# Kernel tuning notes

Hardware: AMD Instinct MI355X
Metric: run time of the kernel (lower is better)

The kernel has to match this reference:

```python
import jax, jax.numpy as jnp
import numpy as np

EMBED_DIM = 1024
NUM_HEADS = 16
HEAD_DIM = EMBED_DIM // NUM_HEADS
SCALE = HEAD_DIM ** -0.5


def setup_inputs() -> dict:
    key = jax.random.key(0)
    ks = jax.random.split(key, 9)
    B, N = 2, 2048
    s = EMBED_DIM ** -0.5  # ~ torch Linear init scale
    x = jax.random.normal(ks[0], (B, N, EMBED_DIM), dtype=jnp.float32)
    Wq = jax.random.uniform(ks[1], (EMBED_DIM, EMBED_DIM), jnp.float32, -s, s)
    bq = jax.random.uniform(ks[2], (EMBED_DIM,), jnp.float32, -s, s)
    Wk = jax.random.uniform(ks[3], (EMBED_DIM, EMBED_DIM), jnp.float32, -s, s)
    bk = jax.random.uniform(ks[4], (EMBED_DIM,), jnp.float32, -s, s)
    Wv = jax.random.uniform(ks[5], (EMBED_DIM, EMBED_DIM), jnp.float32, -s, s)
    bv = jax.random.uniform(ks[6], (EMBED_DIM,), jnp.float32, -s, s)
    Wo = jax.random.uniform(ks[7], (EMBED_DIM, EMBED_DIM), jnp.float32, -s, s)
    bo = jax.random.uniform(ks[8], (EMBED_DIM,), jnp.float32, -s, s)
    return {"x": x, "Wq": Wq, "bq": bq, "Wk": Wk, "bk": bk,
            "Wv": Wv, "bv": bv, "Wo": Wo, "bo": bo}


def reference(x, Wq, bq, Wk, bk, Wv, bv, Wo, bo):
    B, N, R = x.shape
    H, D = NUM_HEADS, HEAD_DIM
    # projections: Linear(x) = x @ W^T + b; reshape to (B, H, N, D)
    def proj(W, b):
        return (x @ W.T + b).reshape(B, N, H, D).transpose(0, 2, 1, 3)
    q = proj(Wq, bq)
    k = proj(Wk, bk)
    v = proj(Wv, bv)
    attn = jnp.einsum('bhnd,bhmd->bhnm', q, k) * SCALE  # (B,H,N,N)
    attn = jax.nn.softmax(attn, axis=-1)
    out = jnp.einsum('bhnm,bhmd->bhnd', attn, v)        # (B,H,N,D)
    out = out.transpose(0, 2, 1, 3).reshape(B, N, R)
    return out @ Wo.T + bo
```

## Files before the change

### kernel.cpp

```cpp
#include <hip/hip_runtime.h>
#include <stdint.h>

typedef __bf16 bf16;
typedef __bf16 bf16x4 __attribute__((ext_vector_type(4)));
typedef __bf16 bf16x8 __attribute__((ext_vector_type(8)));
typedef float f32x4 __attribute__((ext_vector_type(4)));

#define MFMA16(a, b, c) __builtin_amdgcn_mfma_f32_16x16x32_bf16((a), (b), (c), 0, 0, 0)

#define EMBED 1024
#define SEQ   2048
#define MROWS 4096
#define ATTN_QSCALE 0.1803368801111f

__device__ __forceinline__ void gl2lds16(const bf16* g, bf16* l) {
    __builtin_amdgcn_global_load_lds(
        (const __attribute__((address_space(1))) void*)g,
        (__attribute__((address_space(3))) void*)l,
        16, 0, 0);
}

__global__ __launch_bounds__(256) void cast_all_kernel(
    const float* __restrict__ x,  const float* __restrict__ Wq,
    const float* __restrict__ Wk, const float* __restrict__ Wv,
    const float* __restrict__ Wo, bf16* __restrict__ dst) {
    const int blk = blockIdx.x;
    const float* src;
    size_t so, dofs;
    if (blk < 2048) {
        src = x; so = (size_t)blk * 2048; dofs = so;
    } else {
        const int w = (blk - 2048) >> 9;
        so  = (size_t)((blk - 2048) & 511) * 2048;
        src = (w == 0) ? Wq : (w == 1) ? Wk : (w == 2) ? Wv : Wo;
        dofs = (size_t)(4 + w) * 1024 * 1024 + so;
    }
    const size_t i = (size_t)threadIdx.x * 8;
    float4 a = *(const float4*)(src + so + i);
    float4 b = *(const float4*)(src + so + i + 4);
    bf16x8 o;
    o[0] = (bf16)a.x; o[1] = (bf16)a.y; o[2] = (bf16)a.z; o[3] = (bf16)a.w;
    o[4] = (bf16)b.x; o[5] = (bf16)b.y; o[6] = (bf16)b.z; o[7] = (bf16)b.w;
    *(bf16x8*)(dst + dofs + i) = o;
}

template <bool SCALE>
__device__ __forceinline__ void gemm_tile(const bf16* __restrict__ A,
                                          const bf16* __restrict__ W,
                                          const float* __restrict__ bias,
                                          bf16* __restrict__ C,
                                          int m0, int n0, bf16* smem) {
    const int lane = threadIdx.x & 63;
    const int wv   = threadIdx.x >> 6;
    const int wm   = (wv >> 1) * 64;
    const int wn   = (wv & 1) * 64;
    const int fr   = lane & 15;
    const int quad = lane >> 4;
    const int srow = wv * 8 + (lane >> 3);
    const int swz  = (((lane & 7) ^ ((lane >> 3) & 7))) * 8;

    f32x4 acc[4][4];
#pragma unroll
    for (int mt = 0; mt < 4; ++mt)
#pragma unroll
        for (int nt = 0; nt < 4; ++nt)
            acc[mt][nt] = (f32x4){0.f, 0.f, 0.f, 0.f};

    auto stage = [&](int kt, int bb) {
        bf16* As = smem + bb * 16384;
        bf16* Bs = As + 8192;
        const int k0 = kt * 64;
#pragma unroll
        for (int i = 0; i < 4; ++i) {
            gl2lds16(A + (size_t)(m0 + i * 32 + srow) * 1024 + k0 + swz,
                     &As[(i * 32 + wv * 8) * 64]);
            gl2lds16(W + (size_t)(n0 + i * 32 + srow) * 1024 + k0 + swz,
                     &Bs[(i * 32 + wv * 8) * 64]);
        }
    };

    stage(0, 0);
#pragma unroll
    for (int kt = 0; kt < 16; ++kt) {
        const int bb = kt & 1;
        asm volatile("s_waitcnt vmcnt(0)" ::: "memory");
        __builtin_amdgcn_s_barrier();
        if (kt < 15) stage(kt + 1, bb ^ 1);
        const bf16* As = smem + bb * 16384;
        const bf16* Bs = As + 8192;
#pragma unroll
        for (int ks = 0; ks < 2; ++ks) {
            const int fcol = ((ks * 4 + quad) ^ (fr & 7)) * 8;
            bf16x8 af[4], bfr[4];
#pragma unroll
            for (int t = 0; t < 4; ++t) {
                af[t]  = *(const bf16x8*)&As[(wm + t * 16 + fr) * 64 + fcol];
                bfr[t] = *(const bf16x8*)&Bs[(wn + t * 16 + fr) * 64 + fcol];
            }
            __builtin_amdgcn_s_setprio(1);
#pragma unroll
            for (int mt = 0; mt < 4; ++mt)
#pragma unroll
                for (int nt = 0; nt < 4; ++nt)
                    acc[mt][nt] = MFMA16(af[mt], bfr[nt], acc[mt][nt]);
            __builtin_amdgcn_s_setprio(0);
        }
    }

    float bv[4];
#pragma unroll
    for (int nt = 0; nt < 4; ++nt)
        bv[nt] = bias[n0 + wn + nt * 16 + fr];
    const int row4 = quad * 4;
#pragma unroll
    for (int mt = 0; mt < 4; ++mt)
#pragma unroll
        for (int nt = 0; nt < 4; ++nt)
#pragma unroll
            for (int r = 0; r < 4; ++r) {
                int m = m0 + wm + mt * 16 + row4 + r;
                int n = n0 + wn + nt * 16 + fr;
                float v = acc[mt][nt][r] + bv[nt];
                if (SCALE) v *= ATTN_QSCALE;
                C[(size_t)m * 1024 + n] = (bf16)v;
            }
}

__device__ __forceinline__ void v_tile(const bf16* __restrict__ x,
                                       const bf16* __restrict__ Wv,
                                       const float* __restrict__ bias,
                                       bf16* __restrict__ VT,
                                       int m0, int n0, bf16* smem) {
    const int lane = threadIdx.x & 63;
    const int wv   = threadIdx.x >> 6;
    const int wmW  = (wv >> 1) * 64;
    const int wnT  = (wv & 1) * 64;
    const int f    = lane & 15;
    const int quad = lane >> 4;
    const int srow = wv * 8 + (lane >> 3);
    const int swz  = (((lane & 7) ^ ((lane >> 3) & 7))) * 8;

    f32x4 acc[4][4];
#pragma unroll
    for (int mt = 0; mt < 4; ++mt)
#pragma unroll
        for (int nt = 0; nt < 4; ++nt)
            acc[mt][nt] = (f32x4){0.f, 0.f, 0.f, 0.f};

    auto stage = [&](int kt, int bb) {
        bf16* As = smem + bb * 16384;
        bf16* Bs = As + 8192;
        const int k0 = kt * 64;
#pragma unroll
        for (int i = 0; i < 4; ++i) {
            gl2lds16(x  + (size_t)(m0 + i * 32 + srow) * 1024 + k0 + swz,
                     &As[(i * 32 + wv * 8) * 64]);
            gl2lds16(Wv + (size_t)(n0 + i * 32 + srow) * 1024 + k0 + swz,
                     &Bs[(i * 32 + wv * 8) * 64]);
        }
    };

    stage(0, 0);
#pragma unroll
    for (int kt = 0; kt < 16; ++kt) {
        const int bb = kt & 1;
        asm volatile("s_waitcnt vmcnt(0)" ::: "memory");
        __builtin_amdgcn_s_barrier();
        if (kt < 15) stage(kt + 1, bb ^ 1);
        const bf16* As = smem + bb * 16384;
        const bf16* Bs = As + 8192;
#pragma unroll
        for (int ks = 0; ks < 2; ++ks) {
            const int fcol = ((ks * 4 + quad) ^ (f & 7)) * 8;
            bf16x8 wf[4], xf[4];
#pragma unroll
            for (int t = 0; t < 4; ++t) {
                wf[t] = *(const bf16x8*)&Bs[(wmW + t * 16 + f) * 64 + fcol];
                xf[t] = *(const bf16x8*)&As[(wnT + t * 16 + f) * 64 + fcol];
            }
            __builtin_amdgcn_s_setprio(1);
#pragma unroll
            for (int mt = 0; mt < 4; ++mt)
#pragma unroll
                for (int nt = 0; nt < 4; ++nt)
                    acc[mt][nt] = MFMA16(wf[mt], xf[nt], acc[mt][nt]);
            __builtin_amdgcn_s_setprio(0);
        }
    }

    float4 b4[4];
#pragma unroll
    for (int mt = 0; mt < 4; ++mt)
        b4[mt] = *(const float4*)&bias[n0 + wmW + mt * 16 + quad * 4];

    __syncthreads();

#pragma unroll
    for (int mt = 0; mt < 4; ++mt)
#pragma unroll
        for (int nt = 0; nt < 4; ++nt) {
            const int tok = wnT + nt * 16 + f;
#pragma unroll
            for (int r = 0; r < 4; ++r) {
                const float bvr = (r == 0) ? b4[mt].x : (r == 1) ? b4[mt].y
                                : (r == 2) ? b4[mt].z : b4[mt].w;
                smem[(wmW + mt * 16 + quad * 4 + r) * 136 + tok] =
                    (bf16)(acc[mt][nt][r] + bvr);
            }
        }
    __syncthreads();

    const int n_r  = threadIdx.x >> 4;
    const int t8   = (threadIdx.x & 15) * 8;
    const int base = t8 & ~31;
    const int u4   = ((t8 >> 3) & 3) * 4;
    const int bb   = m0 >> 11;
    const int tokg = (m0 & 2047) + t8;
#pragma unroll
    for (int p = 0; p < 8; ++p) {
        const int n_loc = p * 16 + n_r;
        const bf16* row = &smem[n_loc * 136];
        bf16x4 a = *(const bf16x4*)&row[base + u4];
        bf16x4 b = *(const bf16x4*)&row[base + 16 + u4];
        bf16x8 v = {a[0], a[1], a[2], a[3], b[0], b[1], b[2], b[3]};
        *(bf16x8*)&VT[((size_t)(bb * 1024 + n0 + n_loc)) * 2048 + tokg] = v;
    }
}

__global__ __launch_bounds__(256) void qkv_kernel(
    const bf16* __restrict__ x,
    const bf16* __restrict__ Wq, const float* __restrict__ bq,
    const bf16* __restrict__ Wk, const float* __restrict__ bk,
    const bf16* __restrict__ Wv, const float* __restrict__ bv,
    bf16* __restrict__ Q, bf16* __restrict__ K, bf16* __restrict__ VT) {
    __shared__ __align__(16) bf16 smem[32768];
    const int m0    = blockIdx.x * 128;
    const int which = blockIdx.y >> 3;
    const int n0    = (blockIdx.y & 7) * 128;
    if (which == 0)      gemm_tile<true>(x, Wq, bq, Q, m0, n0, smem);
    else if (which == 1) gemm_tile<false>(x, Wk, bk, K, m0, n0, smem);
    else                 v_tile(x, Wv, bv, VT, m0, n0, smem);
}

__global__ __launch_bounds__(256) void oproj_kernel(
    const bf16* __restrict__ A, const bf16* __restrict__ W,
    const float* __restrict__ bias, float* __restrict__ C) {
    const int m0 = blockIdx.x * 128;
    const int n0 = blockIdx.y * 64;

    __shared__ __align__(16) bf16 smem[24576];

    const int lane = threadIdx.x & 63;
    const int wv   = threadIdx.x >> 6;
    const int wm   = (wv >> 1) * 64;
    const int wn   = (wv & 1) * 32;
    const int fr   = lane & 15;
    const int quad = lane >> 4;
    const int srow = wv * 8 + (lane >> 3);
    const int swz  = (((lane & 7) ^ ((lane >> 3) & 7))) * 8;

    f32x4 acc[4][2];
#pragma unroll
    for (int mt = 0; mt < 4; ++mt)
#pragma unroll
        for (int nt = 0; nt < 2; ++nt)
            acc[mt][nt] = (f32x4){0.f, 0.f, 0.f, 0.f};

    auto stage = [&](int kt, int bb) {
        bf16* As = smem + bb * 12288;
        bf16* Bs = As + 8192;
        const int k0 = kt * 64;
#pragma unroll
        for (int i = 0; i < 4; ++i)
            gl2lds16(A + (size_t)(m0 + i * 32 + srow) * 1024 + k0 + swz,
                     &As[(i * 32 + wv * 8) * 64]);
#pragma unroll
        for (int i = 0; i < 2; ++i)
            gl2lds16(W + (size_t)(n0 + i * 32 + srow) * 1024 + k0 + swz,
                     &Bs[(i * 32 + wv * 8) * 64]);
    };

    stage(0, 0);
#pragma unroll
    for (int kt = 0; kt < 16; ++kt) {
        const int bb = kt & 1;
        asm volatile("s_waitcnt vmcnt(0)" ::: "memory");
        __builtin_amdgcn_s_barrier();
        if (kt < 15) stage(kt + 1, bb ^ 1);
        const bf16* As = smem + bb * 12288;
        const bf16* Bs = As + 8192;
#pragma unroll
        for (int ks = 0; ks < 2; ++ks) {
            const int fcol = ((ks * 4 + quad) ^ (fr & 7)) * 8;
            bf16x8 af[4], bfr[2];
#pragma unroll
            for (int t = 0; t < 4; ++t)
                af[t] = *(const bf16x8*)&As[(wm + t * 16 + fr) * 64 + fcol];
#pragma unroll
            for (int t = 0; t < 2; ++t)
                bfr[t] = *(const bf16x8*)&Bs[(wn + t * 16 + fr) * 64 + fcol];
            __builtin_amdgcn_s_setprio(1);
#pragma unroll
            for (int mt = 0; mt < 4; ++mt)
#pragma unroll
                for (int nt = 0; nt < 2; ++nt)
                    acc[mt][nt] = MFMA16(af[mt], bfr[nt], acc[mt][nt]);
            __builtin_amdgcn_s_setprio(0);
        }
    }

    float bv[2];
#pragma unroll
    for (int nt = 0; nt < 2; ++nt)
        bv[nt] = bias[n0 + wn + nt * 16 + fr];
    const int row4 = quad * 4;
#pragma unroll
    for (int mt = 0; mt < 4; ++mt)
#pragma unroll
        for (int nt = 0; nt < 2; ++nt)
#pragma unroll
            for (int r = 0; r < 4; ++r) {
                int m = m0 + wm + mt * 16 + row4 + r;
                int n = n0 + wn + nt * 16 + fr;
                C[(size_t)m * 1024 + n] = acc[mt][nt][r] + bv[nt];
            }
}

__global__ __launch_bounds__(256, 2) void attn_kernel(
    const bf16* __restrict__ Q, const bf16* __restrict__ K,
    const bf16* __restrict__ VT, bf16* __restrict__ Opart,
    float* __restrict__ lpart) {
    const int tid  = threadIdx.x;
    const int lane = tid & 63;
    const int wv   = tid >> 6;
    const int quad = lane >> 4;
    const int f    = lane & 15;
    const int qt   = blockIdx.x >> 1;
    const int half = blockIdx.x & 1;
    const int q0   = qt * 256;
    const int kvb  = half * 1024;
    const int b    = blockIdx.y >> 4;
    const int h    = blockIdx.y & 15;

    const bf16* Qp = Q + ((size_t)b * SEQ) * 1024 + (size_t)h * 64;
    const bf16* Kp = K + ((size_t)b * SEQ) * 1024 + (size_t)h * 64;
    const bf16* Vp = VT + ((size_t)(b * 1024 + h * 64)) * 2048;
    bf16*  Op = Opart + (size_t)half * MROWS * 1024
                      + ((size_t)b * SEQ) * 1024 + (size_t)h * 64;
    float* lp = lpart + ((size_t)(half * 2 + b) * 16 + h) * SEQ;

    __shared__ bf16 Ks[4][64 * 64];
    __shared__ bf16 VTs[4][64 * 64];

    bf16x8 qf[4][2];
#pragma unroll
    for (int qg = 0; qg < 4; ++qg) {
        const bf16* qrow = Qp + (size_t)(q0 + wv * 64 + qg * 16 + f) * 1024;
        qf[qg][0] = *(const bf16x8*)(qrow + quad * 8);
        qf[qg][1] = *(const bf16x8*)(qrow + 32 + quad * 8);
    }

    const int srow = wv * 8 + (lane >> 3);
    const int swz  = (((lane & 7) ^ ((lane >> 3) & 7))) * 8;
    auto stageK = [&](int t, int bb) {
        const int kv0 = kvb + t * 64;
#pragma unroll
        for (int i = 0; i < 2; ++i)
            gl2lds16(Kp + (size_t)(kv0 + i * 32 + srow) * 1024 + swz,
                     &Ks[bb][(i * 32 + wv * 8) * 64]);
    };
    auto stageVT = [&](int t, int bb) {
        const int kv0 = kvb + t * 64;
#pragma unroll
        for (int i = 0; i < 2; ++i)
            gl2lds16(Vp + (size_t)(i * 32 + srow) * 2048 + kv0 + swz,
                     &VTs[bb][(i * 32 + wv * 8) * 64]);
    };

    stageK(0, 0); stageVT(0, 0);
    stageK(1, 1); stageVT(1, 1);

    f32x4 oacc[4][4];
#pragma unroll
    for (int qg = 0; qg < 4; ++qg)
#pragma unroll
        for (int t = 0; t < 4; ++t)
            oacc[qg][t] = (f32x4){0.f, 0.f, 0.f, 0.f};
    f32x4 lacc[4];
#pragma unroll
    for (int qg = 0; qg < 4; ++qg)
        lacc[qg] = (f32x4){0.f, 0.f, 0.f, 0.f};
    const bf16x8 ones8 = {(bf16)1.f, (bf16)1.f, (bf16)1.f, (bf16)1.f,
                          (bf16)1.f, (bf16)1.f, (bf16)1.f, (bf16)1.f};
    const f32x4  zero4 = (f32x4){0.f, 0.f, 0.f, 0.f};

    const int fcol0 = (quad ^ (f & 7)) * 8;
    const int fcol1 = ((4 + quad) ^ (f & 7)) * 8;

    auto step = [&](int t, int bb, int drain) {
        if (drain == 8) { stageK(t + 2, (t + 2) & 3); stageVT(t + 2, (t + 2) & 3); }
        if (drain == 8)      asm volatile("s_waitcnt vmcnt(8)" ::: "memory");
        else if (drain == 4) asm volatile("s_waitcnt vmcnt(4)" ::: "memory");
        else                 asm volatile("s_waitcnt vmcnt(0)" ::: "memory");
        __builtin_amdgcn_s_barrier();

        bf16x8 kf0[4], kf1[4];
#pragma unroll
        for (int t4 = 0; t4 < 4; ++t4) {
            kf0[t4] = *(const bf16x8*)&Ks[bb][(t4 * 16 + f) * 64 + fcol0];
            kf1[t4] = *(const bf16x8*)&Ks[bb][(t4 * 16 + f) * 64 + fcol1];
        }
        bf16x8 pb8[4][2];
#pragma unroll
        for (int qg = 0; qg < 4; ++qg) {
            f32x4 s[4];
            __builtin_amdgcn_s_setprio(1);
#pragma unroll
            for (int t4 = 0; t4 < 4; ++t4) {
                s[t4] = MFMA16(kf0[t4], qf[qg][0], zero4);
                s[t4] = MFMA16(kf1[t4], qf[qg][1], s[t4]);
            }
            __builtin_amdgcn_s_setprio(0);
#pragma unroll
            for (int kt = 0; kt < 2; ++kt) {
#pragma unroll
                for (int r = 0; r < 4; ++r) {
                    pb8[qg][kt][r]     = (bf16)__builtin_amdgcn_exp2f(s[2 * kt][r]);
                    pb8[qg][kt][4 + r] = (bf16)__builtin_amdgcn_exp2f(s[2 * kt + 1][r]);
                }
                lacc[qg] = MFMA16(ones8, pb8[qg][kt], lacc[qg]);
            }
        }

        __builtin_amdgcn_s_setprio(1);
#pragma unroll
        for (int dt = 0; dt < 4; ++dt) {
#pragma unroll
            for (int kt = 0; kt < 2; ++kt) {
                const int pc = ((kt * 4 + quad) ^ (f & 7)) * 8;
                bf16x8 vf = *(const bf16x8*)&VTs[bb][(dt * 16 + f) * 64 + pc];
#pragma unroll
                for (int qg = 0; qg < 4; ++qg)
                    oacc[qg][dt] = MFMA16(vf, pb8[qg][kt], oacc[qg][dt]);
            }
        }
        __builtin_amdgcn_s_setprio(0);
    };

    for (int tt = 0; tt < 12; tt += 4) {
        step(tt, 0, 8); step(tt + 1, 1, 8); step(tt + 2, 2, 8); step(tt + 3, 3, 8);
    }
    step(12, 0, 8); step(13, 1, 8); step(14, 2, 4); step(15, 3, 0);

#pragma unroll
    for (int qg = 0; qg < 4; ++qg) {
        const int q = q0 + wv * 64 + qg * 16 + f;
        bf16* orow = Op + (size_t)q * 1024;
#pragma unroll
        for (int dt = 0; dt < 4; ++dt) {
            bf16x4 ov;
#pragma unroll
            for (int r = 0; r < 4; ++r)
                ov[r] = (bf16)oacc[qg][dt][r];
            *(bf16x4*)(orow + dt * 16 + quad * 4) = ov;
        }
        if (quad == 0)
            lp[q] = lacc[qg][0];
    }
}

__global__ __launch_bounds__(256) void combine_kernel(
    const bf16* __restrict__ Opart, const float* __restrict__ lpart,
    bf16* __restrict__ O) {
    const int gid = blockIdx.x * 256 + threadIdx.x;
    const int row = gid >> 7;
    const int c8  = (gid & 127) * 8;
    const int b   = row >> 11;
    const int tok = row & 2047;
    const int h   = c8 >> 6;

    const float l = lpart[((size_t)(0 * 2 + b) * 16 + h) * SEQ + tok]
                  + lpart[((size_t)(1 * 2 + b) * 16 + h) * SEQ + tok];
    const float inv = 1.0f / l;

    const size_t off = (size_t)row * 1024 + c8;
    bf16x8 a = *(const bf16x8*)&Opart[off];
    bf16x8 c = *(const bf16x8*)&Opart[(size_t)MROWS * 1024 + off];
    bf16x8 o;
#pragma unroll
    for (int i = 0; i < 8; ++i)
        o[i] = (bf16)(((float)a[i] + (float)c[i]) * inv);
    *(bf16x8*)&O[off] = o;
}

extern "C" void kernel_launch(void* const* d_in, const int* in_sizes, int n_in,
                              void* d_out, int out_size, void* d_ws, size_t ws_size,
                              hipStream_t stream) {
    const float* x  = (const float*)d_in[0];
    const float* Wq = (const float*)d_in[1];
    const float* bq = (const float*)d_in[2];
    const float* Wk = (const float*)d_in[3];
    const float* bk = (const float*)d_in[4];
    const float* Wv = (const float*)d_in[5];
    const float* bv = (const float*)d_in[6];
    const float* Wo = (const float*)d_in[7];
    const float* bo = (const float*)d_in[8];
    float* out = (float*)d_out;

    bf16* xb    = (bf16*)d_ws;
    bf16* Wqb   = xb   + (size_t)MROWS * 1024;
    bf16* Wkb   = Wqb  + (size_t)1024 * 1024;
    bf16* Wvb   = Wkb  + (size_t)1024 * 1024;
    bf16* Wob   = Wvb  + (size_t)1024 * 1024;
    bf16* Q     = Wob  + (size_t)1024 * 1024;
    bf16* K     = Q    + (size_t)MROWS * 1024;
    bf16* VT    = K    + (size_t)MROWS * 1024;
    bf16* O     = VT   + (size_t)MROWS * 1024;
    bf16* Opart = O    + (size_t)MROWS * 1024;
    float* lpart = (float*)(Opart + (size_t)2 * MROWS * 1024);

    cast_all_kernel<<<4096, 256, 0, stream>>>(x, Wq, Wk, Wv, Wo, xb);

    qkv_kernel<<<dim3(32, 24), 256, 0, stream>>>(xb, Wqb, bq, Wkb, bk, Wvb, bv, Q, K, VT);
    attn_kernel<<<dim3(16, 32), 256, 0, stream>>>(Q, K, VT, Opart, lpart);
    combine_kernel<<<2048, 256, 0, stream>>>(Opart, lpart, O);
    oproj_kernel<<<dim3(32, 16), 256, 0, stream>>>(O, Wob, bo, out);
}
```

Baseline: 179.9 us.

## Fuse split-KV combine into output projection and swizzle block order for XCDs

Removes the separate combine kernel. The output-projection GEMM now loads both partial attention outputs and their softmax denominators, normalizes them in registers, and writes the A tile to LDS itself. This drops one launch and one write-plus-read of the O buffer. In addition, the qkv, attn and oproj kernels remap the linear block index so that neighbouring tiles land on the same XCD (chiplet), aiming for better L2 reuse. The cost is that the oproj A path now uses register loads instead of async global-to-LDS copies, reads twice as many A bytes per tile, and is recomputed by each of the 16 N-column blocks.

Measured after the change: 188.9 us. 1.05x slower.

```diff
diff --git a/kernel.cpp b/kernel.cpp
--- a/kernel.cpp
+++ b/kernel.cpp
@@ -234,21 +234,27 @@
     const bf16* __restrict__ Wv, const float* __restrict__ bv,
     bf16* __restrict__ Q, bf16* __restrict__ K, bf16* __restrict__ VT) {
     __shared__ __align__(16) bf16 smem[32768];
-    const int m0    = blockIdx.x * 128;
-    const int which = blockIdx.y >> 3;
-    const int n0    = (blockIdx.y & 7) * 128;
+    const int lin   = blockIdx.y * 32 + blockIdx.x;
+    const int sw    = (lin & 7) * 96 + (lin >> 3);
+    const int which = sw >> 8;
+    const int rem   = sw & 255;
+    const int n0    = (rem >> 5) * 128;
+    const int m0    = (rem & 31) * 128;
     if (which == 0)      gemm_tile<true>(x, Wq, bq, Q, m0, n0, smem);
     else if (which == 1) gemm_tile<false>(x, Wk, bk, K, m0, n0, smem);
     else                 v_tile(x, Wv, bv, VT, m0, n0, smem);
 }
 
 __global__ __launch_bounds__(256) void oproj_kernel(
-    const bf16* __restrict__ A, const bf16* __restrict__ W,
-    const float* __restrict__ bias, float* __restrict__ C) {
-    const int m0 = blockIdx.x * 128;
-    const int n0 = blockIdx.y * 64;
-
-    __shared__ __align__(16) bf16 smem[24576];
+    const bf16* __restrict__ Opart, const float* __restrict__ lpart,
+    const bf16* __restrict__ W, const float* __restrict__ bias,
+    float* __restrict__ C) {
+    const int lin = blockIdx.y * 32 + blockIdx.x;
+    const int sw  = (lin & 7) * 64 + (lin >> 3);
+    const int m0  = (sw & 31) * 128;
+    const int n0  = (sw >> 5) * 64;
+
+    __shared__ __align__(16) bf16 smem[2 * 12288];
 
     const int lane = threadIdx.x & 63;
     const int wv   = threadIdx.x >> 6;
@@ -266,27 +272,52 @@
         for (int nt = 0; nt < 2; ++nt)
             acc[mt][nt] = (f32x4){0.f, 0.f, 0.f, 0.f};
 
-    auto stage = [&](int kt, int bb) {
+    bf16x8 a0[4], a1[4];
+    float  l0[4], l1[4];
+
+    auto loadA = [&](int kt) {
+#pragma unroll
+        for (int i = 0; i < 4; ++i) {
+            const int row = m0 + i * 32 + srow;
+            const int b_  = row >> 11;
+            const int tok = row & 2047;
+            const size_t off = (size_t)row * 1024 + kt * 64 + swz;
+            a0[i] = *(const bf16x8*)&Opart[off];
+            a1[i] = *(const bf16x8*)&Opart[(size_t)MROWS * 1024 + off];
+            l0[i] = lpart[((size_t)b_ * 16 + kt) * SEQ + tok];
+            l1[i] = lpart[((size_t)(2 + b_) * 16 + kt) * SEQ + tok];
+        }
+    };
+    auto writeA = [&](int bb) {
         bf16* As = smem + bb * 12288;
-        bf16* Bs = As + 8192;
-        const int k0 = kt * 64;
-#pragma unroll
-        for (int i = 0; i < 4; ++i)
-            gl2lds16(A + (size_t)(m0 + i * 32 + srow) * 1024 + k0 + swz,
-                     &As[(i * 32 + wv * 8) * 64]);
+#pragma unroll
+        for (int i = 0; i < 4; ++i) {
+            const float inv = 1.0f / (l0[i] + l1[i]);
+            bf16x8 o;
+#pragma unroll
+            for (int j = 0; j < 8; ++j)
+                o[j] = (bf16)(((float)a0[i][j] + (float)a1[i][j]) * inv);
+            *(bf16x8*)&As[(i * 32 + srow) * 64 + (lane & 7) * 8] = o;
+        }
+    };
+    auto stageW = [&](int kt, int bb) {
+        bf16* Bs = smem + bb * 12288 + 8192;
 #pragma unroll
         for (int i = 0; i < 2; ++i)
-            gl2lds16(W + (size_t)(n0 + i * 32 + srow) * 1024 + k0 + swz,
+            gl2lds16(W + (size_t)(n0 + i * 32 + srow) * 1024 + kt * 64 + swz,
                      &Bs[(i * 32 + wv * 8) * 64]);
     };
 
-    stage(0, 0);
+    loadA(0);
+    stageW(0, 0);
+    writeA(0);
+    asm volatile("s_waitcnt vmcnt(0) lgkmcnt(0)" ::: "memory");
+    __builtin_amdgcn_s_barrier();
+
 #pragma unroll
     for (int kt = 0; kt < 16; ++kt) {
         const int bb = kt & 1;
-        asm volatile("s_waitcnt vmcnt(0)" ::: "memory");
-        __builtin_amdgcn_s_barrier();
-        if (kt < 15) stage(kt + 1, bb ^ 1);
+        if (kt < 15) { loadA(kt + 1); stageW(kt + 1, bb ^ 1); }
         const bf16* As = smem + bb * 12288;
         const bf16* Bs = As + 8192;
 #pragma unroll
@@ -306,6 +337,11 @@
                 for (int nt = 0; nt < 2; ++nt)
                     acc[mt][nt] = MFMA16(af[mt], bfr[nt], acc[mt][nt]);
             __builtin_amdgcn_s_setprio(0);
+        }
+        if (kt < 15) {
+            writeA(bb ^ 1);
+            asm volatile("s_waitcnt vmcnt(0) lgkmcnt(0)" ::: "memory");
+            __builtin_amdgcn_s_barrier();
         }
     }
 
@@ -335,12 +371,16 @@
     const int wv   = tid >> 6;
     const int quad = lane >> 4;
     const int f    = lane & 15;
-    const int qt   = blockIdx.x >> 1;
-    const int half = blockIdx.x & 1;
+    const int lin  = blockIdx.y * 16 + blockIdx.x;
+    const int sw   = (lin & 7) * 64 + (lin >> 3);
+    const int qh   = sw & 15;
+    const int bh   = sw >> 4;
+    const int qt   = qh >> 1;
+    const int half = qh & 1;
     const int q0   = qt * 256;
     const int kvb  = half * 1024;
-    const int b    = blockIdx.y >> 4;
-    const int h    = blockIdx.y & 15;
+    const int b    = bh >> 4;
+    const int h    = bh & 15;
 
     const bf16* Qp = Q + ((size_t)b * SEQ) * 1024 + (size_t)h * 64;
     const bf16* Kp = K + ((size_t)b * SEQ) * 1024 + (size_t)h * 64;
@@ -467,30 +507,6 @@
         if (quad == 0)
             lp[q] = lacc[qg][0];
     }
-}
-
-__global__ __launch_bounds__(256) void combine_kernel(
-    const bf16* __restrict__ Opart, const float* __restrict__ lpart,
-    bf16* __restrict__ O) {
-    const int gid = blockIdx.x * 256 + threadIdx.x;
-    const int row = gid >> 7;
-    const int c8  = (gid & 127) * 8;
-    const int b   = row >> 11;
-    const int tok = row & 2047;
-    const int h   = c8 >> 6;
-
-    const float l = lpart[((size_t)(0 * 2 + b) * 16 + h) * SEQ + tok]
-                  + lpart[((size_t)(1 * 2 + b) * 16 + h) * SEQ + tok];
-    const float inv = 1.0f / l;
-
-    const size_t off = (size_t)row * 1024 + c8;
-    bf16x8 a = *(const bf16x8*)&Opart[off];
-    bf16x8 c = *(const bf16x8*)&Opart[(size_t)MROWS * 1024 + off];
-    bf16x8 o;
-#pragma unroll
-    for (int i = 0; i < 8; ++i)
-        o[i] = (bf16)(((float)a[i] + (float)c[i]) * inv);
-    *(bf16x8*)&O[off] = o;
 }
 
 extern "C" void kernel_launch(void* const* d_in, const int* in_sizes, int n_in,
@@ -515,14 +531,12 @@
     bf16* Q     = Wob  + (size_t)1024 * 1024;
     bf16* K     = Q    + (size_t)MROWS * 1024;
     bf16* VT    = K    + (size_t)MROWS * 1024;
-    bf16* O     = VT   + (size_t)MROWS * 1024;
-    bf16* Opart = O    + (size_t)MROWS * 1024;
+    bf16* Opart = VT   + (size_t)MROWS * 1024;
     float* lpart = (float*)(Opart + (size_t)2 * MROWS * 1024);
 
     cast_all_kernel<<<4096, 256, 0, stream>>>(x, Wq, Wk, Wv, Wo, xb);
 
     qkv_kernel<<<dim3(32, 24), 256, 0, stream>>>(xb, Wqb, bq, Wkb, bk, Wvb, bv, Q, K, VT);
     attn_kernel<<<dim3(16, 32), 256, 0, stream>>>(Q, K, VT, Opart, lpart);
-    combine_kernel<<<2048, 256, 0, stream>>>(Opart, lpart, O);
-    oproj_kernel<<<dim3(32, 16), 256, 0, stream>>>(O, Wob, bo, out);
-}
+    oproj_kernel<<<dim3(32, 16), 256, 0, stream>>>(Opart, lpart, Wob, bo, out);
+}
```

## Software-pipeline QK^T of next tile with PV of current tile and swizzle block order

Applied to the files above, without the earlier changes.

Restructures the attention inner loop so each step computes the QK^T scores and exp for tile t+1 while doing the PV MFMAs for tile t, with double-buffered probability registers (pbA/pbB) and a prologue/epilogue. It also remaps the block index so that consecutive blocks are spread across heads and batches, which may change how K/V reuse lands in L2. The aim is to let the exp/VALU work overlap with matrix-core work and to improve cache locality. In exchange it raises register pressure, which could cause spills at 2 waves per SIMD, and the waitcnt accounting is changed to one tile of lookahead.

Result: faster. 175.8 us (-2.3%).

```diff
diff --git a/kernel.cpp b/kernel.cpp
--- a/kernel.cpp
+++ b/kernel.cpp
@@ -335,12 +335,16 @@
     const int wv   = tid >> 6;
     const int quad = lane >> 4;
     const int f    = lane & 15;
-    const int qt   = blockIdx.x >> 1;
-    const int half = blockIdx.x & 1;
+    const int lin  = blockIdx.y * 16 + blockIdx.x;
+    const int sw   = (lin & 7) * 64 + (lin >> 3);
+    const int qh   = sw & 15;
+    const int bh   = sw >> 4;
+    const int qt   = qh >> 1;
+    const int half = qh & 1;
     const int q0   = qt * 256;
     const int kvb  = half * 1024;
-    const int b    = blockIdx.y >> 4;
-    const int h    = blockIdx.y & 15;
+    const int b    = bh >> 4;
+    const int h    = bh & 15;
 
     const bf16* Qp = Q + ((size_t)b * SEQ) * 1024 + (size_t)h * 64;
     const bf16* Kp = K + ((size_t)b * SEQ) * 1024 + (size_t)h * 64;
@@ -397,20 +401,17 @@
     const int fcol0 = (quad ^ (f & 7)) * 8;
     const int fcol1 = ((4 + quad) ^ (f & 7)) * 8;
 
-    auto step = [&](int t, int bb, int drain) {
-        if (drain == 8) { stageK(t + 2, (t + 2) & 3); stageVT(t + 2, (t + 2) & 3); }
-        if (drain == 8)      asm volatile("s_waitcnt vmcnt(8)" ::: "memory");
-        else if (drain == 4) asm volatile("s_waitcnt vmcnt(4)" ::: "memory");
-        else                 asm volatile("s_waitcnt vmcnt(0)" ::: "memory");
-        __builtin_amdgcn_s_barrier();
-
+    bf16x8 pbA[4][2], pbB[4][2];
+
+    asm volatile("s_waitcnt vmcnt(4)" ::: "memory");
+    __builtin_amdgcn_s_barrier();
+    {
         bf16x8 kf0[4], kf1[4];
 #pragma unroll
         for (int t4 = 0; t4 < 4; ++t4) {
-            kf0[t4] = *(const bf16x8*)&Ks[bb][(t4 * 16 + f) * 64 + fcol0];
-            kf1[t4] = *(const bf16x8*)&Ks[bb][(t4 * 16 + f) * 64 + fcol1];
-        }
-        bf16x8 pb8[4][2];
+            kf0[t4] = *(const bf16x8*)&Ks[0][(t4 * 16 + f) * 64 + fcol0];
+            kf1[t4] = *(const bf16x8*)&Ks[0][(t4 * 16 + f) * 64 + fcol1];
+        }
 #pragma unroll
         for (int qg = 0; qg < 4; ++qg) {
             f32x4 s[4];
@@ -425,32 +426,73 @@
             for (int kt = 0; kt < 2; ++kt) {
 #pragma unroll
                 for (int r = 0; r < 4; ++r) {
-                    pb8[qg][kt][r]     = (bf16)__builtin_amdgcn_exp2f(s[2 * kt][r]);
-                    pb8[qg][kt][4 + r] = (bf16)__builtin_amdgcn_exp2f(s[2 * kt + 1][r]);
+                    pbA[qg][kt][r]     = (bf16)__builtin_amdgcn_exp2f(s[2 * kt][r]);
+                    pbA[qg][kt][4 + r] = (bf16)__builtin_amdgcn_exp2f(s[2 * kt + 1][r]);
                 }
-                lacc[qg] = MFMA16(ones8, pb8[qg][kt], lacc[qg]);
-            }
-        }
-
-        __builtin_amdgcn_s_setprio(1);
-#pragma unroll
-        for (int dt = 0; dt < 4; ++dt) {
+                lacc[qg] = MFMA16(ones8, pbA[qg][kt], lacc[qg]);
+            }
+        }
+    }
+
+    auto step = [&](int t, bf16x8 (&pbc)[4][2], bf16x8 (&pbn)[4][2],
+                    int drain, bool doStage, bool doQK) {
+        if (doStage) { stageK(t + 2, (t + 2) & 3); stageVT(t + 2, (t + 2) & 3); }
+        if (drain == 4) asm volatile("s_waitcnt vmcnt(4)" ::: "memory");
+        else            asm volatile("s_waitcnt vmcnt(0)" ::: "memory");
+        __builtin_amdgcn_s_barrier();
+        const int bq = (t + 1) & 3;
+        const int bp = t & 3;
+
+        bf16x8 kf0[4], kf1[4];
+        if (doQK) {
+#pragma unroll
+            for (int t4 = 0; t4 < 4; ++t4) {
+                kf0[t4] = *(const bf16x8*)&Ks[bq][(t4 * 16 + f) * 64 + fcol0];
+                kf1[t4] = *(const bf16x8*)&Ks[bq][(t4 * 16 + f) * 64 + fcol1];
+            }
+        }
+#pragma unroll
+        for (int u = 0; u < 4; ++u) {
+            f32x4 s[4];
+            if (doQK) {
+                __builtin_amdgcn_s_setprio(1);
+#pragma unroll
+                for (int t4 = 0; t4 < 4; ++t4) {
+                    s[t4] = MFMA16(kf0[t4], qf[u][0], zero4);
+                    s[t4] = MFMA16(kf1[t4], qf[u][1], s[t4]);
+                }
+                __builtin_amdgcn_s_setprio(0);
+            }
+            __builtin_amdgcn_s_setprio(1);
 #pragma unroll
             for (int kt = 0; kt < 2; ++kt) {
                 const int pc = ((kt * 4 + quad) ^ (f & 7)) * 8;
-                bf16x8 vf = *(const bf16x8*)&VTs[bb][(dt * 16 + f) * 64 + pc];
+                bf16x8 vf = *(const bf16x8*)&VTs[bp][(u * 16 + f) * 64 + pc];
 #pragma unroll
                 for (int qg = 0; qg < 4; ++qg)
-                    oacc[qg][dt] = MFMA16(vf, pb8[qg][kt], oacc[qg][dt]);
-            }
-        }
-        __builtin_amdgcn_s_setprio(0);
+                    oacc[qg][u] = MFMA16(vf, pbc[qg][kt], oacc[qg][u]);
+            }
+            __builtin_amdgcn_s_setprio(0);
+            if (doQK) {
+#pragma unroll
+                for (int kt = 0; kt < 2; ++kt) {
+#pragma unroll
+                    for (int r = 0; r < 4; ++r) {
+                        pbn[u][kt][r]     = (bf16)__builtin_amdgcn_exp2f(s[2 * kt][r]);
+                        pbn[u][kt][4 + r] = (bf16)__builtin_amdgcn_exp2f(s[2 * kt + 1][r]);
+                    }
+                    lacc[u] = MFMA16(ones8, pbn[u][kt], lacc[u]);
+                }
+            }
+        }
     };
 
-    for (int tt = 0; tt < 12; tt += 4) {
-        step(tt, 0, 8); step(tt + 1, 1, 8); step(tt + 2, 2, 8); step(tt + 3, 3, 8);
-    }
-    step(12, 0, 8); step(13, 1, 8); step(14, 2, 4); step(15, 3, 0);
+    for (int tt = 0; tt < 14; tt += 2) {
+        step(tt,     pbA, pbB, 4, true, true);
+        step(tt + 1, pbB, pbA, 4, true, true);
+    }
+    step(14, pbA, pbB, 0, false, true);
+    step(15, pbB, pbA, 0, false, false);
 
 #pragma unroll
     for (int qg = 0; qg < 4; ++qg) {
```
